# Kernel optimization log

Measured on AMD Instinct MI355X. Metric: run time of the kernel, lower is better.

Reference implementation:

```python
import jax, jax.numpy as jnp
import numpy as np

N, E, DIN, H = 100000, 1600000, 128, 128


def gcn_conv(x, W, b, row, col, ew, n):
    """PyG GCNConv with add_self_loops=True, symmetric normalization.

    deg[i] = sum of edge weights into i (col) + 1 (self loop weight).
    norm_e = deg^{-1/2}[row_e] * ew_e * deg^{-1/2}[col_e]
    out[col] += norm_e * (x @ W)[row]; self-loop contributes deg^{-1}[i] * xw[i].
    """
    xw = x @ W  # [n, H]
    deg = jax.ops.segment_sum(ew, col, num_segments=n) + 1.0  # self-loop weight 1
    dinv = jax.lax.rsqrt(deg)  # deg >= 1 so safe
    norm = dinv[row] * ew * dinv[col]  # [E]
    agg = jax.ops.segment_sum(norm[:, None] * xw[row], col, num_segments=n)
    agg = agg + (dinv * dinv)[:, None] * xw  # self loops
    return agg + b


def setup_inputs() -> dict:
    key = jax.random.key(0)
    ks = jax.random.split(key, 9)
    x = jax.random.normal(ks[0], (N, DIN), jnp.float32)
    edge_index = jax.random.randint(ks[1], (2, E), 0, N, dtype=jnp.int64)
    edge_attr = jax.random.uniform(ks[2], (E,), jnp.float32)
    s_in = 1.0 / np.sqrt(DIN)
    s_h = 1.0 / np.sqrt(H)
    W1 = jax.random.normal(ks[3], (DIN, H), jnp.float32) * s_in
    b1 = jnp.zeros((H,), jnp.float32)
    W2 = jax.random.normal(ks[4], (H, H), jnp.float32) * s_h
    b2 = jnp.zeros((H,), jnp.float32)
    W3 = jax.random.normal(ks[5], (H, H), jnp.float32) * s_h
    b3 = jnp.zeros((H,), jnp.float32)
    return {"x": x, "edge_index": edge_index, "edge_attr": edge_attr,
            "W1": W1, "b1": b1, "W2": W2, "b2": b2, "W3": W3, "b3": b3}


def reference(x, edge_index, edge_attr, W1, b1, W2, b2, W3, b3):
    row, col = edge_index[0], edge_index[1]
    n = x.shape[0]
    h = jax.nn.relu(gcn_conv(x, W1, b1, row, col, edge_attr, n))
    h = jax.nn.relu(gcn_conv(h, W2, b2, row, col, edge_attr, n))
    h = jax.nn.relu(gcn_conv(h, W3, b3, row, col, edge_attr, n))
    return h
```

## Files before the change

### kernel.cpp

```cpp
#include <hip/hip_runtime.h>
#include <hip/hip_fp16.h>

#define CAP 64
#define BSH 7
#define BCAP 2560
#define NBMAX 1024

typedef _Float16 half8 __attribute__((ext_vector_type(8)));
typedef float f32x4 __attribute__((ext_vector_type(4)));


__global__ __launch_bounds__(256) void k_init(int* gcur, int nbkt) {
    int i = blockIdx.x * 256 + threadIdx.x;
    if (i < nbkt) gcur[i] = 0;
}

__global__ __launch_bounds__(256) void k_bucket(const int* __restrict__ row,
                                                const int* __restrict__ col,
                                                const float* __restrict__ ew,
                                                int* gcur, int2* sortedE,
                                                int e, int nbkt) {
    __shared__ int lcnt[NBMAX];
    __shared__ int lbase[NBMAX];
    int tid = threadIdx.x;
    for (int b = tid; b < nbkt; b += 256) lcnt[b] = 0;
    __syncthreads();
    int base = blockIdx.x * 2048;
    int bk[8], rk[8], rx[8], rwi[8];
#pragma unroll
    for (int u = 0; u < 8; ++u) {
        int i = base + tid + u * 256;
        bk[u] = -1;
        if (i < e) {
            int c = col[i];
            bk[u] = c >> BSH;
            rx[u] = row[i] | ((c & ((1 << BSH) - 1)) << 17);
            rwi[u] = __float_as_int(ew[i]);
            rk[u] = atomicAdd(&lcnt[bk[u]], 1);
        }
    }
    __syncthreads();
    for (int b = tid; b < nbkt; b += 256) {
        int c = lcnt[b];
        lbase[b] = c ? atomicAdd(&gcur[b], c) : 0;
    }
    __syncthreads();
#pragma unroll
    for (int u = 0; u < 8; ++u) {
        if (bk[u] >= 0) {
            int pos = lbase[bk[u]] + rk[u];
            if (pos < BCAP) sortedE[(long)bk[u] * BCAP + pos] = make_int2(rx[u], rwi[u]);
        }
    }
}

__global__ __launch_bounds__(256) void k_csr(const int2* __restrict__ sortedE,
                                             const int* __restrict__ gcur,
                                             int2* __restrict__ csr,
                                             int* __restrict__ counts,
                                             float* __restrict__ dinv, int n) {
    int bkt = blockIdx.x;
    __shared__ int c128[128];
    __shared__ float s128[128];
    int tid = threadIdx.x;
    if (tid < 128) { c128[tid] = 0; s128[tid] = 0.f; }
    __syncthreads();
    int cnt = gcur[bkt];
    if (cnt > BCAP) cnt = BCAP;
    for (int j = tid; j < cnt; j += 256) {
        int2 rec = sortedE[(long)bkt * BCAP + j];
        int cl = rec.x >> 17;
        int r0 = rec.x & 0x1FFFF;
        float w = __int_as_float(rec.y);
        int r = atomicAdd(&c128[cl], 1);
        if (r < CAP) csr[((long)((bkt << BSH) + cl)) * CAP + r] = make_int2(r0, rec.y);
        atomicAdd(&s128[cl], w);
    }
    __syncthreads();
    if (tid < 128) {
        int node = (bkt << BSH) + tid;
        if (node < n) {
            int c = c128[tid];
            counts[node] = c < CAP ? c : CAP;
            dinv[node] = rsqrtf(s128[tid] + 1.0f);
        }
    }
}

__global__ __launch_bounds__(256) void k_norm(const int* __restrict__ counts,
                                              const float* __restrict__ dinv,
                                              int2* csr, int n) {
    int gw = (blockIdx.x * 256 + threadIdx.x) >> 6;
    int lane = threadIdx.x & 63;
    if (gw >= n) return;
    int cnt = __builtin_amdgcn_readfirstlane(counts[gw]);
    float dc = dinv[gw];
    if (lane < cnt) {
        long idx = (long)gw * CAP + lane;
        int2 ent = csr[idx];
        float w = dinv[ent.x] * __int_as_float(ent.y) * dc;
        csr[idx] = make_int2(ent.x, __float_as_int(w));
    }
}

__global__ __launch_bounds__(256) void k_wt(const float* __restrict__ W1,
                                            const float* __restrict__ W2,
                                            const float* __restrict__ W3,
                                            __half* __restrict__ Wt) {
    int m = blockIdx.x >> 6;
    int kb = (blockIdx.x & 63) << 1;
    const float* W = m == 0 ? W1 : (m == 1 ? W2 : W3);
    __half* T = Wt + (long)m * 16384;
    int k = kb + (threadIdx.x >> 7);
    int nn = threadIdx.x & 127;
    T[nn * 128 + k] = __float2half(W[k * 128 + nn]);
}


__global__ __launch_bounds__(256) void k_gemm(const float* __restrict__ Xf,
                                              const __half* __restrict__ Xh,
                                              const __half* __restrict__ Wt,
                                              __half* __restrict__ Yh, int n) {
    __shared__ __half Wl[128 * 128];
    int tid = threadIdx.x;
    {
        const uint4* src = (const uint4*)Wt;
#pragma unroll
        for (int i = 0; i < 8; ++i) {
            int c = tid + 256 * i;
            int nrow = c >> 4, k8 = c & 15;
            uint4 v = src[c];
            int byte = nrow * 256 + ((k8 * 16) ^ ((nrow & 7) << 4));
            *(uint4*)((char*)Wl + byte) = v;
        }
    }
    __syncthreads();
    int wid = tid >> 6, lane = tid & 63;
    int l16 = lane & 15, lq = lane >> 4;
    long row0 = (long)blockIdx.x * 128 + wid * 32;
    f32x4 acc[2][8] = {};
#pragma unroll
    for (int ks = 0; ks < 4; ++ks) {
        int k0 = ks * 32;
        half8 a[2];
#pragma unroll
        for (int mt = 0; mt < 2; ++mt) {
            long r = row0 + mt * 16 + l16;
            if (r >= n) r = n - 1;
            if (Xf) {
                const float* px = Xf + r * 128 + k0 + lq * 8;
                float4 f0 = *(const float4*)px;
                float4 f1 = *(const float4*)(px + 4);
                half8 h;
                h[0] = (_Float16)f0.x; h[1] = (_Float16)f0.y;
                h[2] = (_Float16)f0.z; h[3] = (_Float16)f0.w;
                h[4] = (_Float16)f1.x; h[5] = (_Float16)f1.y;
                h[6] = (_Float16)f1.z; h[7] = (_Float16)f1.w;
                a[mt] = h;
            } else {
                a[mt] = *(const half8*)(Xh + r * 128 + k0 + lq * 8);
            }
        }
#pragma unroll
        for (int nt = 0; nt < 8; ++nt) {
            int nrow = nt * 16 + l16;
            int byte = nrow * 256 + (((k0 + lq * 8) * 2) ^ ((nrow & 7) << 4));
            half8 b = *(const half8*)((char*)Wl + byte);
            acc[0][nt] = __builtin_amdgcn_mfma_f32_16x16x32_f16(a[0], b, acc[0][nt], 0, 0, 0);
            acc[1][nt] = __builtin_amdgcn_mfma_f32_16x16x32_f16(a[1], b, acc[1][nt], 0, 0, 0);
        }
    }
#pragma unroll
    for (int mt = 0; mt < 2; ++mt) {
#pragma unroll
        for (int r = 0; r < 4; ++r) {
            long rw = row0 + mt * 16 + lq * 4 + r;
            if (rw < n) {
#pragma unroll
                for (int nt = 0; nt < 8; ++nt) {
                    Yh[rw * 128 + nt * 16 + l16] = __float2half(acc[mt][nt][r]);
                }
            }
        }
    }
}

__global__ __launch_bounds__(256) void k_agg(const int2* __restrict__ csr,
                                             const int* __restrict__ counts,
                                             const float* __restrict__ dinv,
                                             const __half* __restrict__ xwh,
                                             const float* __restrict__ bias,
                                             __half* __restrict__ outh,
                                             float* __restrict__ outf, int n) {
    int gw = (blockIdx.x * 256 + threadIdx.x) >> 6;
    int lane = threadIdx.x & 63;
    if (gw >= n) return;
    int cnt = __builtin_amdgcn_readfirstlane(counts[gw]);
    const __half2* xh2 = (const __half2*)xwh;
    float ax = 0.f, ay = 0.f;
    int2 ent = make_int2(gw, 0);
    if (lane < cnt) ent = csr[(long)gw * CAP + lane];
    int mr = (cnt + 15) & ~15;
    for (int j = 0; j < mr; j += 16) {
        int rr[16];
        __half2 hh[16];
        float ww[16];
#pragma unroll
        for (int u = 0; u < 16; ++u) rr[u] = __shfl(ent.x, j + u);
#pragma unroll
        for (int u = 0; u < 16; ++u) hh[u] = xh2[(long)rr[u] * 64 + lane];
#pragma unroll
        for (int u = 0; u < 16; ++u) ww[u] = __int_as_float(__shfl(ent.y, j + u));
#pragma unroll
        for (int u = 0; u < 16; ++u) {
            float2 v = __half22float2(hh[u]);
            ax = fmaf(ww[u], v.x, ax);
            ay = fmaf(ww[u], v.y, ay);
        }
    }
    float di = dinv[gw];
    float d2 = di * di;
    float2 sv = __half22float2(xh2[(long)gw * 64 + lane]);
    float2 bv = ((const float2*)bias)[lane];
    float ox = fmaxf(ax + d2 * sv.x + bv.x, 0.f);
    float oy = fmaxf(ay + d2 * sv.y + bv.y, 0.f);
    if (outh) {
        __half2 ho = __floats2half2_rn(ox, oy);
        ((__half2*)outh)[(long)gw * 64 + lane] = ho;
    }
    if (outf) {
        ((float2*)outf)[(long)gw * 64 + lane] = make_float2(ox, oy);
    }
}


extern "C" void kernel_launch(void* const* d_in, const int* in_sizes, int n_in,
                              void* d_out, int out_size, void* d_ws, size_t ws_size,
                              hipStream_t stream) {
    const float* x  = (const float*)d_in[0];
    const int*   ei = (const int*)d_in[1];
    const float* ew = (const float*)d_in[2];
    const float* W1 = (const float*)d_in[3];
    const float* b1 = (const float*)d_in[4];
    const float* W2 = (const float*)d_in[5];
    const float* b2 = (const float*)d_in[6];
    const float* W3 = (const float*)d_in[7];
    const float* b3 = (const float*)d_in[8];

    const int n = in_sizes[0] / 128;
    const int e = in_sizes[2];
    const int* row = ei;
    const int* col = ei + e;
    const int nbkt = (n + (1 << BSH) - 1) >> BSH;

    char* p = (char*)d_ws;
    auto alloc = [&](size_t bytes) {
        char* q = p;
        p += (bytes + 255) & ~(size_t)255;
        return q;
    };
    int*    gcur    = (int*)alloc((size_t)nbkt * 4);
    int*    counts  = (int*)alloc((size_t)n * 4);
    float*  dinv    = (float*)alloc((size_t)n * 4);
    __half* Wt      = (__half*)alloc((size_t)3 * 16384 * 2);
    int2*   sortedE = (int2*)alloc((size_t)nbkt * BCAP * 8);
    int2*   csr     = (int2*)alloc((size_t)n * CAP * 8);
    __half* xwh     = (__half*)alloc((size_t)n * 128 * 2);
    __half* h       = (__half*)alloc((size_t)n * 128 * 2);
    (void)ws_size; (void)n_in; (void)out_size;

    int gb = (n + 127) / 128;
    int ab = ((size_t)n * 64 + 255) / 256;
    int sb = (e + 2047) / 2048;

    k_init  <<<(nbkt + 255) / 256, 256, 0, stream>>>(gcur, nbkt);
    k_bucket<<<sb, 256, 0, stream>>>(row, col, ew, gcur, sortedE, e, nbkt);
    k_csr   <<<nbkt, 256, 0, stream>>>(sortedE, gcur, csr, counts, dinv, n);
    k_norm  <<<ab, 256, 0, stream>>>(counts, dinv, csr, n);
    k_wt    <<<192, 256, 0, stream>>>(W1, W2, W3, Wt);

    k_gemm<<<gb, 256, 0, stream>>>(x, (const __half*)nullptr, Wt, xwh, n);
    k_agg <<<ab, 256, 0, stream>>>(csr, counts, dinv, xwh, b1, h, (float*)nullptr, n);
    k_gemm<<<gb, 256, 0, stream>>>((const float*)nullptr, h, Wt + 16384, xwh, n);
    k_agg <<<ab, 256, 0, stream>>>(csr, counts, dinv, xwh, b2, h, (float*)nullptr, n);
    k_gemm<<<gb, 256, 0, stream>>>((const float*)nullptr, h, Wt + 32768, xwh, n);
    k_agg <<<ab, 256, 0, stream>>>(csr, counts, dinv, xwh, b3, (__half*)nullptr, (float*)d_out, n);
}
```

Before: 322.4 us.

## Split CSR into row/half-weight arrays and gather 32 neighbors unconditionally

```diff
diff --git a/kernel.cpp b/kernel.cpp
--- a/kernel.cpp
+++ b/kernel.cpp
@@ -56,7 +56,8 @@
 
 __global__ __launch_bounds__(256) void k_csr(const int2* __restrict__ sortedE,
                                              const int* __restrict__ gcur,
-                                             int2* __restrict__ csr,
+                                             int* __restrict__ rowsA,
+                                             float* __restrict__ wraw,
                                              int* __restrict__ counts,
                                              float* __restrict__ dinv, int n) {
     int bkt = blockIdx.x;
@@ -73,7 +74,11 @@
         int r0 = rec.x & 0x1FFFF;
         float w = __int_as_float(rec.y);
         int r = atomicAdd(&c128[cl], 1);
-        if (r < CAP) csr[((long)((bkt << BSH) + cl)) * CAP + r] = make_int2(r0, rec.y);
+        if (r < CAP) {
+            long idx = ((long)((bkt << BSH) + cl)) * CAP + r;
+            rowsA[idx] = r0;
+            wraw[idx] = w;
+        }
         atomicAdd(&s128[cl], w);
     }
     __syncthreads();
@@ -89,7 +94,9 @@
 
 __global__ __launch_bounds__(256) void k_norm(const int* __restrict__ counts,
                                               const float* __restrict__ dinv,
-                                              int2* csr, int n) {
+                                              const int* __restrict__ rowsA,
+                                              const float* __restrict__ wraw,
+                                              __half* __restrict__ wh, int n) {
     int gw = (blockIdx.x * 256 + threadIdx.x) >> 6;
     int lane = threadIdx.x & 63;
     if (gw >= n) return;
@@ -97,9 +104,8 @@
     float dc = dinv[gw];
     if (lane < cnt) {
         long idx = (long)gw * CAP + lane;
-        int2 ent = csr[idx];
-        float w = dinv[ent.x] * __int_as_float(ent.y) * dc;
-        csr[idx] = make_int2(ent.x, __float_as_int(w));
+        float w = dinv[rowsA[idx]] * wraw[idx] * dc;
+        wh[idx] = __float2half(w);
     }
 }
 
@@ -185,7 +191,8 @@
     }
 }
 
-__global__ __launch_bounds__(256) void k_agg(const int2* __restrict__ csr,
+__global__ __launch_bounds__(256) void k_agg(const int* __restrict__ rowsA,
+                                             const __half* __restrict__ wh,
                                              const int* __restrict__ counts,
                                              const float* __restrict__ dinv,
                                              const __half* __restrict__ xwh,
@@ -197,31 +204,48 @@
     if (gw >= n) return;
     int cnt = __builtin_amdgcn_readfirstlane(counts[gw]);
     const __half2* xh2 = (const __half2*)xwh;
-    float ax = 0.f, ay = 0.f;
-    int2 ent = make_int2(gw, 0);
-    if (lane < cnt) ent = csr[(long)gw * CAP + lane];
-    int mr = (cnt + 15) & ~15;
-    for (int j = 0; j < mr; j += 16) {
-        int rr[16];
-        __half2 hh[16];
-        float ww[16];
-#pragma unroll
-        for (int u = 0; u < 16; ++u) rr[u] = __shfl(ent.x, j + u);
-#pragma unroll
-        for (int u = 0; u < 16; ++u) hh[u] = xh2[(long)rr[u] * 64 + lane];
-#pragma unroll
-        for (int u = 0; u < 16; ++u) ww[u] = __int_as_float(__shfl(ent.y, j + u));
-#pragma unroll
-        for (int u = 0; u < 16; ++u) {
-            float2 v = __half22float2(hh[u]);
-            ax = fmaf(ww[u], v.x, ax);
-            ay = fmaf(ww[u], v.y, ay);
-        }
-    }
-    float di = dinv[gw];
-    float d2 = di * di;
     float2 sv = __half22float2(xh2[(long)gw * 64 + lane]);
     float2 bv = ((const float2*)bias)[lane];
+    float di = dinv[gw];
+    int r_ent = gw;
+    float w_ent = 0.f;
+    if (lane < cnt) {
+        long idx = (long)gw * CAP + lane;
+        r_ent = rowsA[idx];
+        w_ent = __half2float(wh[idx]);
+    }
+    float ax = 0.f, ay = 0.f;
+    {
+        __half2 hh[32];
+#pragma unroll
+        for (int u = 0; u < 32; ++u) {
+            int r = __shfl(r_ent, u);
+            hh[u] = xh2[(long)r * 64 + lane];
+        }
+#pragma unroll
+        for (int u = 0; u < 32; ++u) {
+            float w = __shfl(w_ent, u);
+            float2 v = __half22float2(hh[u]);
+            ax = fmaf(w, v.x, ax);
+            ay = fmaf(w, v.y, ay);
+        }
+    }
+    if (cnt > 32) {
+        __half2 hh[32];
+#pragma unroll
+        for (int u = 0; u < 32; ++u) {
+            int r = __shfl(r_ent, 32 + u);
+            hh[u] = xh2[(long)r * 64 + lane];
+        }
+#pragma unroll
+        for (int u = 0; u < 32; ++u) {
+            float w = __shfl(w_ent, 32 + u);
+            float2 v = __half22float2(hh[u]);
+            ax = fmaf(w, v.x, ax);
+            ay = fmaf(w, v.y, ay);
+        }
+    }
+    float d2 = di * di;
     float ox = fmaxf(ax + d2 * sv.x + bv.x, 0.f);
     float oy = fmaxf(ay + d2 * sv.y + bv.y, 0.f);
     if (outh) {
@@ -264,7 +288,9 @@
     float*  dinv    = (float*)alloc((size_t)n * 4);
     __half* Wt      = (__half*)alloc((size_t)3 * 16384 * 2);
     int2*   sortedE = (int2*)alloc((size_t)nbkt * BCAP * 8);
-    int2*   csr     = (int2*)alloc((size_t)n * CAP * 8);
+    int*    rowsA   = (int*)alloc((size_t)n * CAP * 4);
+    float*  wraw    = (float*)alloc((size_t)n * CAP * 4);
+    __half* wh      = (__half*)alloc((size_t)n * CAP * 2);
     __half* xwh     = (__half*)alloc((size_t)n * 128 * 2);
     __half* h       = (__half*)alloc((size_t)n * 128 * 2);
     (void)ws_size; (void)n_in; (void)out_size;
@@ -275,14 +301,14 @@
 
     k_init  <<<(nbkt + 255) / 256, 256, 0, stream>>>(gcur, nbkt);
     k_bucket<<<sb, 256, 0, stream>>>(row, col, ew, gcur, sortedE, e, nbkt);
-    k_csr   <<<nbkt, 256, 0, stream>>>(sortedE, gcur, csr, counts, dinv, n);
-    k_norm  <<<ab, 256, 0, stream>>>(counts, dinv, csr, n);
+    k_csr   <<<nbkt, 256, 0, stream>>>(sortedE, gcur, rowsA, wraw, counts, dinv, n);
+    k_norm  <<<ab, 256, 0, stream>>>(counts, dinv, rowsA, wraw, wh, n);
     k_wt    <<<192, 256, 0, stream>>>(W1, W2, W3, Wt);
 
     k_gemm<<<gb, 256, 0, stream>>>(x, (const __half*)nullptr, Wt, xwh, n);
-    k_agg <<<ab, 256, 0, stream>>>(csr, counts, dinv, xwh, b1, h, (float*)nullptr, n);
+    k_agg <<<ab, 256, 0, stream>>>(rowsA, wh, counts, dinv, xwh, b1, h, (float*)nullptr, n);
     k_gemm<<<gb, 256, 0, stream>>>((const float*)nullptr, h, Wt + 16384, xwh, n);
-    k_agg <<<ab, 256, 0, stream>>>(csr, counts, dinv, xwh, b2, h, (float*)nullptr, n);
+    k_agg <<<ab, 256, 0, stream>>>(rowsA, wh, counts, dinv, xwh, b2, h, (float*)nullptr, n);
     k_gemm<<<gb, 256, 0, stream>>>((const float*)nullptr, h, Wt + 32768, xwh, n);
-    k_agg <<<ab, 256, 0, stream>>>(csr, counts, dinv, xwh, b3, (__half*)nullptr, (float*)d_out, n);
-}
+    k_agg <<<ab, 256, 0, stream>>>(rowsA, wh, counts, dinv, xwh, b3, (__half*)nullptr, (float*)d_out, n);
+}
```

Result: slower. 341.5 us (+5.9%).

## Gather four neighbor rows per wave with 16-byte loads in aggregation

Applied to the files above, without the earlier changes.

```diff
diff --git a/kernel.cpp b/kernel.cpp
--- a/kernel.cpp
+++ b/kernel.cpp
@@ -196,40 +196,60 @@
     int lane = threadIdx.x & 63;
     if (gw >= n) return;
     int cnt = __builtin_amdgcn_readfirstlane(counts[gw]);
-    const __half2* xh2 = (const __half2*)xwh;
-    float ax = 0.f, ay = 0.f;
+    int g = lane >> 4;
+    int c16 = lane & 15;
+    float di = dinv[gw];
+    half8 sv8 = *(const half8*)(xwh + (long)gw * 128 + c16 * 8);
+    float4 bv0 = *(const float4*)(bias + c16 * 8);
+    float4 bv1 = *(const float4*)(bias + c16 * 8 + 4);
     int2 ent = make_int2(gw, 0);
     if (lane < cnt) ent = csr[(long)gw * CAP + lane];
+    float acc[8] = {};
     int mr = (cnt + 15) & ~15;
     for (int j = 0; j < mr; j += 16) {
-        int rr[16];
-        __half2 hh[16];
-        float ww[16];
-#pragma unroll
-        for (int u = 0; u < 16; ++u) rr[u] = __shfl(ent.x, j + u);
-#pragma unroll
-        for (int u = 0; u < 16; ++u) hh[u] = xh2[(long)rr[u] * 64 + lane];
-#pragma unroll
-        for (int u = 0; u < 16; ++u) ww[u] = __int_as_float(__shfl(ent.y, j + u));
-#pragma unroll
-        for (int u = 0; u < 16; ++u) {
-            float2 v = __half22float2(hh[u]);
-            ax = fmaf(ww[u], v.x, ax);
-            ay = fmaf(ww[u], v.y, ay);
-        }
-    }
-    float di = dinv[gw];
+        half8 hv[4];
+        float wv[4];
+#pragma unroll
+        for (int q = 0; q < 4; ++q) {
+            int r = __shfl(ent.x, j + q * 4 + g);
+            hv[q] = *(const half8*)(xwh + (long)r * 128 + c16 * 8);
+        }
+#pragma unroll
+        for (int q = 0; q < 4; ++q) wv[q] = __int_as_float(__shfl(ent.y, j + q * 4 + g));
+#pragma unroll
+        for (int q = 0; q < 4; ++q) {
+#pragma unroll
+            for (int t = 0; t < 8; ++t) acc[t] = fmaf(wv[q], (float)hv[q][t], acc[t]);
+        }
+    }
+#pragma unroll
+    for (int t = 0; t < 8; ++t) {
+        acc[t] += __shfl_xor(acc[t], 16);
+        acc[t] += __shfl_xor(acc[t], 32);
+    }
     float d2 = di * di;
-    float2 sv = __half22float2(xh2[(long)gw * 64 + lane]);
-    float2 bv = ((const float2*)bias)[lane];
-    float ox = fmaxf(ax + d2 * sv.x + bv.x, 0.f);
-    float oy = fmaxf(ay + d2 * sv.y + bv.y, 0.f);
-    if (outh) {
-        __half2 ho = __floats2half2_rn(ox, oy);
-        ((__half2*)outh)[(long)gw * 64 + lane] = ho;
-    }
-    if (outf) {
-        ((float2*)outf)[(long)gw * 64 + lane] = make_float2(ox, oy);
+    float o[8];
+    o[0] = fmaxf(acc[0] + d2 * (float)sv8[0] + bv0.x, 0.f);
+    o[1] = fmaxf(acc[1] + d2 * (float)sv8[1] + bv0.y, 0.f);
+    o[2] = fmaxf(acc[2] + d2 * (float)sv8[2] + bv0.z, 0.f);
+    o[3] = fmaxf(acc[3] + d2 * (float)sv8[3] + bv0.w, 0.f);
+    o[4] = fmaxf(acc[4] + d2 * (float)sv8[4] + bv1.x, 0.f);
+    o[5] = fmaxf(acc[5] + d2 * (float)sv8[5] + bv1.y, 0.f);
+    o[6] = fmaxf(acc[6] + d2 * (float)sv8[6] + bv1.z, 0.f);
+    o[7] = fmaxf(acc[7] + d2 * (float)sv8[7] + bv1.w, 0.f);
+    if (g == 0) {
+        if (outh) {
+            half8 ho;
+#pragma unroll
+            for (int t = 0; t < 8; ++t) ho[t] = (_Float16)o[t];
+            *(half8*)(outh + (long)gw * 128 + c16 * 8) = ho;
+        }
+        if (outf) {
+            float4 f0 = make_float4(o[0], o[1], o[2], o[3]);
+            float4 f1 = make_float4(o[4], o[5], o[6], o[7]);
+            *(float4*)(outf + (long)gw * 128 + c16 * 8) = f0;
+            *(float4*)(outf + (long)gw * 128 + c16 * 8 + 4) = f1;
+        }
     }
 }
 
```

Measured after the change: 316.5 us. No clear change (-1.8%).
